# Optimization experiments

Measured on AMD Instinct MI355X. Metric: run time of the kernel, lower is better.

Reference implementation:

```python
import jax, jax.numpy as jnp
import numpy as np

N = 16384  # number of paired examples
D = 1024   # encoder hidden size


def setup_inputs() -> dict:
    key = jax.random.key(0)
    kx, ky = jax.random.split(key)
    x = jax.random.normal(kx, (N, D), dtype=jnp.float32)
    y = jax.random.normal(ky, (N, D), dtype=jnp.float32)
    return {"x": x, "y": y}


def reference(x, y):
    # Original: (x @ y.T).diagonal(). The diagonal of the Gram matrix is the
    # row-wise dot product, computed directly without the O(N^2 d) GEMM.
    return jnp.einsum("nd,nd->n", x, y)
```

## Files before the change

kernel.cpp:

```cpp
#include <hip/hip_runtime.h>


#define D 1024

__global__ __launch_bounds__(256, 4) void rowdot_kernel(const float* __restrict__ x,
                                                        const float* __restrict__ y,
                                                        float* __restrict__ out) {
    const int wave = threadIdx.x >> 6;
    const int lane = threadIdx.x & 63;
    const int row0 = (blockIdx.x * 4 + wave) * 4;

    #pragma unroll
    for (int i = 0; i < 4; i += 2) {
        const int r = row0 + i;
        const float4* __restrict__ xr0 = (const float4*)(x + (size_t)r * D);
        const float4* __restrict__ yr0 = (const float4*)(y + (size_t)r * D);
        const float4* __restrict__ xr1 = (const float4*)(x + (size_t)(r + 1) * D);
        const float4* __restrict__ yr1 = (const float4*)(y + (size_t)(r + 1) * D);

        float4 a[4], b[4], c[4], d[4];
        #pragma unroll
        for (int j = 0; j < 4; ++j) a[j] = xr0[lane + 64 * j];
        #pragma unroll
        for (int j = 0; j < 4; ++j) b[j] = yr0[lane + 64 * j];
        #pragma unroll
        for (int j = 0; j < 4; ++j) c[j] = xr1[lane + 64 * j];
        #pragma unroll
        for (int j = 0; j < 4; ++j) d[j] = yr1[lane + 64 * j];

        float s0 = 0.0f, s1 = 0.0f;
        #pragma unroll
        for (int j = 0; j < 4; ++j) {
            s0 += a[j].x * b[j].x + a[j].y * b[j].y + a[j].z * b[j].z + a[j].w * b[j].w;
            s1 += c[j].x * d[j].x + c[j].y * d[j].y + c[j].z * d[j].z + c[j].w * d[j].w;
        }

        #pragma unroll
        for (int off = 32; off > 0; off >>= 1) {
            s0 += __shfl_down(s0, off, 64);
            s1 += __shfl_down(s1, off, 64);
        }

        if (lane == 0) {
            *(float2*)(out + r) = make_float2(s0, s1);
        }
    }
}

extern "C" void kernel_launch(void* const* d_in, const int* in_sizes, int n_in,
                              void* d_out, int out_size, void* d_ws, size_t ws_size,
                              hipStream_t stream) {
    const float* x = (const float*)d_in[0];
    const float* y = (const float*)d_in[1];
    float* out = (float*)d_out;
    const int N = out_size;

    rowdot_kernel<<<N / 16, 256, 0, stream>>>(x, y, out);
}
```

Before: 144.4 us.

## Double-buffer row-pair loads in registers and process eight rows per wave

Each wave now handles eight rows instead of four and holds two register buffers. The loads for the next row pair are issued before the current pair is reduced, with compiler memory barriers fixing that order, so memory latency overlaps with compute. The grid is halved and the min-blocks launch bound is removed, which raises register use and may lower occupancy. The input stream is memory-bound, so the gain depends on whether the deeper per-wave memory-level parallelism makes up for fewer waves in flight.

```diff
diff --git a/kernel.cpp b/kernel.cpp
--- a/kernel.cpp
+++ b/kernel.cpp
@@ -3,48 +3,70 @@
 
 #define D 1024
 
-__global__ __launch_bounds__(256, 4) void rowdot_kernel(const float* __restrict__ x,
-                                                        const float* __restrict__ y,
-                                                        float* __restrict__ out) {
+typedef float v4f __attribute__((ext_vector_type(4)));
+
+__device__ __forceinline__ void load_pair(const float* __restrict__ x,
+                                          const float* __restrict__ y,
+                                          int row, int lane, v4f R[16]) {
+    const v4f* __restrict__ x0 = (const v4f*)(x + (size_t)row * D);
+    const v4f* __restrict__ y0 = (const v4f*)(y + (size_t)row * D);
+    const v4f* __restrict__ x1 = (const v4f*)(x + (size_t)(row + 1) * D);
+    const v4f* __restrict__ y1 = (const v4f*)(y + (size_t)(row + 1) * D);
+    #pragma unroll
+    for (int j = 0; j < 4; ++j) R[j]      = x0[lane + 64 * j];
+    #pragma unroll
+    for (int j = 0; j < 4; ++j) R[4 + j]  = y0[lane + 64 * j];
+    #pragma unroll
+    for (int j = 0; j < 4; ++j) R[8 + j]  = x1[lane + 64 * j];
+    #pragma unroll
+    for (int j = 0; j < 4; ++j) R[12 + j] = y1[lane + 64 * j];
+}
+
+__device__ __forceinline__ void reduce_store_pair(float* __restrict__ out,
+                                                  int row, int lane,
+                                                  const v4f R[16]) {
+    float s0 = 0.0f, s1 = 0.0f;
+    #pragma unroll
+    for (int j = 0; j < 4; ++j) {
+        s0 += R[j].x * R[4 + j].x + R[j].y * R[4 + j].y +
+              R[j].z * R[4 + j].z + R[j].w * R[4 + j].w;
+        s1 += R[8 + j].x * R[12 + j].x + R[8 + j].y * R[12 + j].y +
+              R[8 + j].z * R[12 + j].z + R[8 + j].w * R[12 + j].w;
+    }
+    #pragma unroll
+    for (int off = 32; off > 0; off >>= 1) {
+        s0 += __shfl_down(s0, off, 64);
+        s1 += __shfl_down(s1, off, 64);
+    }
+    if (lane == 0) {
+        *(float2*)(out + row) = make_float2(s0, s1);
+    }
+}
+
+#define PIN() asm volatile("" ::: "memory")
+
+__global__ __launch_bounds__(256) void rowdot_kernel(const float* __restrict__ x,
+                                                     const float* __restrict__ y,
+                                                     float* __restrict__ out) {
     const int wave = threadIdx.x >> 6;
     const int lane = threadIdx.x & 63;
-    const int row0 = (blockIdx.x * 4 + wave) * 4;
+    const int w = blockIdx.x * 4 + wave;
+    const int r = w * 8;
 
-    #pragma unroll
-    for (int i = 0; i < 4; i += 2) {
-        const int r = row0 + i;
-        const float4* __restrict__ xr0 = (const float4*)(x + (size_t)r * D);
-        const float4* __restrict__ yr0 = (const float4*)(y + (size_t)r * D);
-        const float4* __restrict__ xr1 = (const float4*)(x + (size_t)(r + 1) * D);
-        const float4* __restrict__ yr1 = (const float4*)(y + (size_t)(r + 1) * D);
+    v4f A[16], B[16];
 
-        float4 a[4], b[4], c[4], d[4];
-        #pragma unroll
-        for (int j = 0; j < 4; ++j) a[j] = xr0[lane + 64 * j];
-        #pragma unroll
-        for (int j = 0; j < 4; ++j) b[j] = yr0[lane + 64 * j];
-        #pragma unroll
-        for (int j = 0; j < 4; ++j) c[j] = xr1[lane + 64 * j];
-        #pragma unroll
-        for (int j = 0; j < 4; ++j) d[j] = yr1[lane + 64 * j];
-
-        float s0 = 0.0f, s1 = 0.0f;
-        #pragma unroll
-        for (int j = 0; j < 4; ++j) {
-            s0 += a[j].x * b[j].x + a[j].y * b[j].y + a[j].z * b[j].z + a[j].w * b[j].w;
-            s1 += c[j].x * d[j].x + c[j].y * d[j].y + c[j].z * d[j].z + c[j].w * d[j].w;
-        }
-
-        #pragma unroll
-        for (int off = 32; off > 0; off >>= 1) {
-            s0 += __shfl_down(s0, off, 64);
-            s1 += __shfl_down(s1, off, 64);
-        }
-
-        if (lane == 0) {
-            *(float2*)(out + r) = make_float2(s0, s1);
-        }
-    }
+    load_pair(x, y, r + 0, lane, A);
+    load_pair(x, y, r + 2, lane, B);
+    PIN();
+    reduce_store_pair(out, r + 0, lane, A);
+    load_pair(x, y, r + 4, lane, A);
+    PIN();
+    reduce_store_pair(out, r + 2, lane, B);
+    load_pair(x, y, r + 6, lane, B);
+    PIN();
+    reduce_store_pair(out, r + 4, lane, A);
+    PIN();
+    reduce_store_pair(out, r + 6, lane, B);
 }
 
 extern "C" void kernel_launch(void* const* d_in, const int* in_sizes, int n_in,
@@ -55,5 +77,5 @@
     float* out = (float*)d_out;
     const int N = out_size;
 
-    rowdot_kernel<<<N / 16, 256, 0, stream>>>(x, y, out);
+    rowdot_kernel<<<N / 32, 256, 0, stream>>>(x, y, out);
 }
```

Result: no change. 143.3 us (-0.8%).
